# Kernel optimization log

Hardware: AMD Instinct MI355X
Metric: run time of the kernel (lower is better)

## Reference

```python
import jax, jax.numpy as jnp
import numpy as np

B = 16
N = [20000, 5000, 1250, 313, 79]          # node counts per pooling level (fine -> coarse)
E = [120000, 30000, 7500, 1878, 474]      # ~6 edges per node (triangle mesh)
FILTERS = [3, 32, 32, 64, 64, 64]
K = 6
Z = 64
COND = 2
N_LAYERS = 4


def setup_inputs():
    ks = iter(jax.random.split(jax.random.key(0), 64))
    inp = {}
    inp["x"] = jax.random.normal(next(ks), (B * N[0], FILTERS[0]), jnp.float32)
    inp["label"] = jax.random.normal(next(ks), (B, COND), jnp.float32)
    for i in range(5):
        inp[f"edges{i}"] = jax.random.randint(next(ks), (2, E[i]), 0, N[i])
    for i in range(4):
        inp[f"ds_idx{i}"] = jax.random.randint(next(ks), (N[i + 1],), 0, N[i])
        inp[f"us_idx{i}"] = jax.random.randint(next(ks), (N[i], 3), 0, N[i + 1])
        inp[f"us_w{i}"] = jax.random.uniform(next(ks), (N[i], 3), jnp.float32)
    for i in range(4):
        inp[f"enc_w{i}"] = 0.1 * jax.random.normal(next(ks), (K, FILTERS[i], FILTERS[i + 1]), jnp.float32)
        inp[f"enc_b{i}"] = 0.1 * jax.random.normal(next(ks), (FILTERS[i + 1],), jnp.float32)
    for i in range(5):
        inp[f"dec_w{i}"] = 0.1 * jax.random.normal(next(ks), (K, FILTERS[-i - 1], FILTERS[-i - 2]), jnp.float32)
    for i in range(4):
        inp[f"dec_b{i}"] = 0.1 * jax.random.normal(next(ks), (FILTERS[-i - 2],), jnp.float32)
    lat_in = N[4] * FILTERS[-1]
    inp["enc_mu_w"] = 0.1 * jax.random.normal(next(ks), (lat_in, Z), jnp.float32)
    inp["enc_mu_b"] = jnp.zeros((Z,), jnp.float32)
    inp["enc_lv_w"] = 0.1 * jax.random.normal(next(ks), (lat_in, Z), jnp.float32)
    inp["enc_lv_b"] = jnp.zeros((Z,), jnp.float32)
    inp["dec_lin_w"] = 0.1 * jax.random.normal(next(ks), (Z + COND, lat_in), jnp.float32)
    inp["dec_lin_b"] = jnp.zeros((lat_in,), jnp.float32)
    return inp


def _sym_norm(edges, n):
    # ChebConv_Coma.norm: norm = D^-1/2[row] * w * D^-1/2[col], unit weights
    row, col = edges[0], edges[1]
    deg = jnp.zeros((n,), jnp.float32).at[row].add(1.0)
    dinv = jnp.where(deg > 0, deg ** -0.5, 0.0)
    return dinv[row] * dinv[col]


def _cheb(x, edges, norm, W, b):
    # Chebyshev recursion: Tx_0=x, Tx_1=L~x, Tx_k=2 L~ Tx_{k-1} - Tx_{k-2}
    src, tgt = edges[0], edges[1]

    def prop(h):  # h: [B, Nn, F] -> scatter-sum of norm-weighted source features
        return jnp.zeros_like(h).at[:, tgt].add(h[:, src] * norm[None, :, None])

    Tx0 = x
    out = jnp.einsum('bnf,fg->bng', Tx0, W[0])
    Tx1 = prop(x)
    out = out + jnp.einsum('bnf,fg->bng', Tx1, W[1])
    for k in range(2, W.shape[0]):
        Tx2 = 2.0 * prop(Tx1) - Tx0
        out = out + jnp.einsum('bnf,fg->bng', Tx2, W[k])
        Tx0, Tx1 = Tx1, Tx2
    return out if b is None else out + b


def _forward(x, label, us_ws, enc_ws, enc_bs, dec_ws, dec_bs,
             enc_mu_w, enc_mu_b, enc_lv_w, enc_lv_b, dec_lin_w, dec_lin_b,
             edges, norms, ds_idx, us_idx):
    h = x.reshape(B, N[0], FILTERS[0])
    # encoder
    for i in range(N_LAYERS):
        h = jax.nn.relu(_cheb(h, edges[i], norms[i], enc_ws[i], enc_bs[i]))
        h = h[:, ds_idx[i]]  # binary downsample matrix == row gather
    h = h.reshape(B, N[4] * FILTERS[-1])
    mu = h @ enc_mu_w + enc_mu_b
    logvar = h @ enc_lv_w + enc_lv_b
    # reparameterize (fixed eps for determinism)
    eps = jax.random.normal(jax.random.key(42), mu.shape, mu.dtype)
    z = mu + eps * jnp.exp(0.5 * logvar)
    # decoder
    h = jnp.concatenate([z, label], axis=1)
    h = jax.nn.relu(h @ dec_lin_w + dec_lin_b).reshape(B, N[4], FILTERS[-1])
    for i in range(N_LAYERS):
        lvl = N_LAYERS - 1 - i
        # barycentric upsample: 3 nonzeros per output row
        h = jnp.einsum('rk,brkf->brf', us_ws[lvl], h[:, us_idx[lvl]])
        h = jax.nn.relu(_cheb(h, edges[lvl], norms[lvl], dec_ws[i], dec_bs[i]))
    # faithful quirk of the original: final conv uses A_edge_index[-1] (coarsest graph edges)
    h = _cheb(h, edges[-1], norms[-1], dec_ws[4], None)
    return h.reshape(-1, FILTERS[0]), mu, logvar


def reference(x, label,
              edges0, edges1, edges2, edges3, edges4,
              ds_idx0, ds_idx1, ds_idx2, ds_idx3,
              us_idx0, us_idx1, us_idx2, us_idx3,
              us_w0, us_w1, us_w2, us_w3,
              enc_w0, enc_w1, enc_w2, enc_w3,
              enc_b0, enc_b1, enc_b2, enc_b3,
              dec_w0, dec_w1, dec_w2, dec_w3, dec_w4,
              dec_b0, dec_b1, dec_b2, dec_b3,
              enc_mu_w, enc_mu_b, enc_lv_w, enc_lv_b, dec_lin_w, dec_lin_b):
    edges = [edges0, edges1, edges2, edges3, edges4]
    norms = [_sym_norm(edges[i], N[i]) for i in range(5)]
    return _forward(x, label,
                    [us_w0, us_w1, us_w2, us_w3],
                    [enc_w0, enc_w1, enc_w2, enc_w3],
                    [enc_b0, enc_b1, enc_b2, enc_b3],
                    [dec_w0, dec_w1, dec_w2, dec_w3, dec_w4],
                    [dec_b0, dec_b1, dec_b2, dec_b3],
                    enc_mu_w, enc_mu_b, enc_lv_w, enc_lv_b, dec_lin_w, dec_lin_b,
                    edges, norms,
                    [ds_idx0, ds_idx1, ds_idx2, ds_idx3],
                    [us_idx0, us_idx1, us_idx2, us_idx3])
```

## Files before the change

kernel.cpp:

```cpp
#include <hip/hip_runtime.h>
#include <cstdint>
#include <cstddef>

#define WG 256
#define NB 16


struct IP5 { const int* e[5]; };
struct Ptr3 { const float* p[3]; };


__global__ void k_zero_i(int* __restrict__ p, int n) {
  int i = blockIdx.x * WG + threadIdx.x;
  if (i < n) p[i] = 0;
}

__global__ void k_hist_all(IP5 ep, int* __restrict__ dsrc, int* __restrict__ dtgt) {
  int i = blockIdx.x * WG + threadIdx.x;
  if (i >= 159852) return;
  int l, eo, ee, no, co;
  if (i < 120000)      { l = 0; eo = 0;      ee = 120000; no = 0;     co = 0; }
  else if (i < 150000) { l = 1; eo = 120000; ee = 30000;  no = 20000; co = 20000; }
  else if (i < 157500) { l = 2; eo = 150000; ee = 7500;   no = 25000; co = 25000; }
  else if (i < 159378) { l = 3; eo = 157500; ee = 1878;   no = 26250; co = 26250; }
  else                 { l = 4; eo = 159378; ee = 474;    no = 26563; co = 26563; }
  int e = i - eo;
  const int* E = ep.e[l];
  atomicAdd(&dsrc[no + E[e]], 1);
  atomicAdd(&dtgt[co + E[ee + e]], 1);
}

__global__ void k_scan_all(const int* __restrict__ deg_all, int* __restrict__ rowptr_all,
                           int* __restrict__ cursor_all) {
  static const int Ns[5] = {20000, 5000, 1250, 313, 20000};
  static const int CO[5] = {0, 20000, 25000, 26250, 26563};
  static const int RO[5] = {0, 20001, 25002, 26253, 26567};
  __shared__ int s[WG];
  int l = blockIdx.x;
  int N = Ns[l];
  const int* deg = deg_all + CO[l];
  int* rowptr = rowptr_all + RO[l];
  int* cursor = cursor_all + CO[l];
  int t = threadIdx.x;
  int chunk = (N + WG - 1) / WG;
  int a = t * chunk;
  int b = min(N, a + chunk);
  int sum = 0;
  for (int i = a; i < b; i++) sum += deg[i];
  s[t] = sum;
  __syncthreads();
  for (int off = 1; off < WG; off <<= 1) {
    int v = (t >= off) ? s[t - off] : 0;
    __syncthreads();
    s[t] += v;
    __syncthreads();
  }
  int run = (t == 0) ? 0 : s[t - 1];
  for (int i = a; i < b; i++) {
    rowptr[i] = run;
    cursor[i] = run;
    run += deg[i];
  }
  if (t == 0) rowptr[N] = s[WG - 1];
}


static __device__ __forceinline__ float erfinv_f(float x) {
  float w = -log1pf(-x * x);
  float p;
  if (w < 5.0f) {
    w -= 2.5f;
    p = 2.81022636e-08f;
    p = fmaf(p, w, 3.43273939e-07f);
    p = fmaf(p, w, -3.5233877e-06f);
    p = fmaf(p, w, -4.39150654e-06f);
    p = fmaf(p, w, 0.00021858087f);
    p = fmaf(p, w, -0.00125372503f);
    p = fmaf(p, w, -0.00417768164f);
    p = fmaf(p, w, 0.246640727f);
    p = fmaf(p, w, 1.50140941f);
  } else {
    w = sqrtf(w) - 3.0f;
    p = -0.000200214257f;
    p = fmaf(p, w, 0.000100950558f);
    p = fmaf(p, w, 0.00134934322f);
    p = fmaf(p, w, -0.00367342844f);
    p = fmaf(p, w, 0.00573950773f);
    p = fmaf(p, w, -0.0076224613f);
    p = fmaf(p, w, 0.00943887047f);
    p = fmaf(p, w, 1.00167406f);
    p = fmaf(p, w, 2.83297682f);
  }
  return p * x;
}

static __device__ __forceinline__ float bits_to_normal(unsigned b) {
  float f = __uint_as_float((b >> 9) | 0x3f800000u) - 1.0f;
  const float lo = -0.99999994f;
  float u = f * (1.0f - lo) + lo;
  u = fmaxf(u, lo);
  return 1.41421356f * erfinv_f(u);
}

static __device__ __forceinline__ float eps_val(int i) {
  unsigned x0 = 0u, x1 = (unsigned)i;
  unsigned ks[3] = {0u, 42u, 0u ^ 42u ^ 0x1BD11BDAu};
  x0 += ks[0];
  x1 += ks[1];
  const int R[2][4] = {{13, 15, 26, 6}, {17, 29, 16, 24}};
#pragma unroll
  for (int it = 0; it < 5; it++) {
#pragma unroll
    for (int j = 0; j < 4; j++) {
      x0 += x1;
      int r = R[it & 1][j];
      x1 = (x1 << r) | (x1 >> (32 - r));
      x1 ^= x0;
    }
    x0 += ks[(it + 1) % 3];
    x1 += ks[(it + 2) % 3] + (unsigned)(it + 1);
  }
  return bits_to_normal(x0 ^ x1);
}

__global__ void k_fill_all(IP5 ep, const int* __restrict__ dsrc, int* __restrict__ cursor,
                           int* __restrict__ csrc, float* __restrict__ csw,
                           float* __restrict__ eps, const float* __restrict__ x,
                           float* __restrict__ sxl) {
  int blk = blockIdx.x;
  if (blk < 625) {
    int i = blk * WG + threadIdx.x;
    if (i >= 159852) return;
    int l, eo, ee, no, co, eb;
    if (i < 120000)      { l = 0; eo = 0;      ee = 120000; no = 0;     co = 0;     eb = 0; }
    else if (i < 150000) { l = 1; eo = 120000; ee = 30000;  no = 20000; co = 20000; eb = 120000; }
    else if (i < 157500) { l = 2; eo = 150000; ee = 7500;   no = 25000; co = 25000; eb = 150000; }
    else if (i < 159378) { l = 3; eo = 157500; ee = 1878;   no = 26250; co = 26250; eb = 157500; }
    else                 { l = 4; eo = 159378; ee = 474;    no = 26563; co = 26563; eb = 159378; }
    int e = i - eo;
    const int* E = ep.e[l];
    int s = E[e], t = E[ee + e];
    float da = (float)dsrc[no + s], db = (float)dsrc[no + t];
    float wa = (da > 0.f) ? (1.0f / sqrtf(da)) : 0.f;
    float wb = (db > 0.f) ? (1.0f / sqrtf(db)) : 0.f;
    int pos = atomicAdd(&cursor[co + t], 1);
    csrc[eb + pos] = s;
    csw[eb + pos] = wa * wb;
  } else if (blk < 629) {
    int j = (blk - 625) * WG + threadIdx.x;
    if (j < 1024) eps[j] = eps_val(j);
  } else {
    int j = (blk - 629) * WG + threadIdx.x;
    if (j >= NB * 20000 * 3) return;
    int f = j % 3;
    int b = (j / 3) % NB;
    int n = j / 48;
    sxl[j] = x[((size_t)b * 20000 + n) * 3 + f];
  }
}


#define RFL_I(v) __builtin_amdgcn_readfirstlane(v)
#define RFL_F(v) __int_as_float(__builtin_amdgcn_readfirstlane(__float_as_int(v)))

template <int F>
__global__ __launch_bounds__(WG) void k_propw(const float* __restrict__ in,
                                              float* __restrict__ out,
                                              const float* __restrict__ sub, float scale,
                                              const int* __restrict__ rowptr,
                                              const int* __restrict__ csrc,
                                              const float* __restrict__ csw, int N) {
  constexpr int C4 = F / 16;
  int node = blockIdx.x * 4 + (threadIdx.x >> 6);
  if (node >= N) return;
  int lane = threadIdx.x & 63;
  const float4* in4 = (const float4*)in;
  float4 acc[C4];
#pragma unroll
  for (int u = 0; u < C4; u++) acc[u] = make_float4(0.f, 0.f, 0.f, 0.f);
  int beg = rowptr[node], end = rowptr[node + 1];
  int j = beg;
  for (; j + 3 < end; j += 4) {
    int s0 = RFL_I(csrc[j]);
    int s1 = RFL_I(csrc[j + 1]);
    int s2 = RFL_I(csrc[j + 2]);
    int s3 = RFL_I(csrc[j + 3]);
    float w0 = RFL_F(csw[j]);
    float w1 = RFL_F(csw[j + 1]);
    float w2 = RFL_F(csw[j + 2]);
    float w3 = RFL_F(csw[j + 3]);
    const float4* p0 = in4 + (size_t)s0 * (4 * F) + lane;
    const float4* p1 = in4 + (size_t)s1 * (4 * F) + lane;
    const float4* p2 = in4 + (size_t)s2 * (4 * F) + lane;
    const float4* p3 = in4 + (size_t)s3 * (4 * F) + lane;
    float4 v0[C4], v1[C4], v2[C4], v3[C4];
#pragma unroll
    for (int u = 0; u < C4; u++) v0[u] = p0[u * 64];
#pragma unroll
    for (int u = 0; u < C4; u++) v1[u] = p1[u * 64];
#pragma unroll
    for (int u = 0; u < C4; u++) v2[u] = p2[u * 64];
#pragma unroll
    for (int u = 0; u < C4; u++) v3[u] = p3[u * 64];
#pragma unroll
    for (int u = 0; u < C4; u++) {
      acc[u].x = fmaf(w0, v0[u].x, acc[u].x); acc[u].y = fmaf(w0, v0[u].y, acc[u].y);
      acc[u].z = fmaf(w0, v0[u].z, acc[u].z); acc[u].w = fmaf(w0, v0[u].w, acc[u].w);
      acc[u].x = fmaf(w1, v1[u].x, acc[u].x); acc[u].y = fmaf(w1, v1[u].y, acc[u].y);
      acc[u].z = fmaf(w1, v1[u].z, acc[u].z); acc[u].w = fmaf(w1, v1[u].w, acc[u].w);
      acc[u].x = fmaf(w2, v2[u].x, acc[u].x); acc[u].y = fmaf(w2, v2[u].y, acc[u].y);
      acc[u].z = fmaf(w2, v2[u].z, acc[u].z); acc[u].w = fmaf(w2, v2[u].w, acc[u].w);
      acc[u].x = fmaf(w3, v3[u].x, acc[u].x); acc[u].y = fmaf(w3, v3[u].y, acc[u].y);
      acc[u].z = fmaf(w3, v3[u].z, acc[u].z); acc[u].w = fmaf(w3, v3[u].w, acc[u].w);
    }
  }
  for (; j < end; j++) {
    int s0 = RFL_I(csrc[j]);
    float w0 = RFL_F(csw[j]);
    const float4* p0 = in4 + (size_t)s0 * (4 * F) + lane;
#pragma unroll
    for (int u = 0; u < C4; u++) {
      float4 v0 = p0[u * 64];
      acc[u].x = fmaf(w0, v0.x, acc[u].x); acc[u].y = fmaf(w0, v0.y, acc[u].y);
      acc[u].z = fmaf(w0, v0.z, acc[u].z); acc[u].w = fmaf(w0, v0.w, acc[u].w);
    }
  }
  float4* o4 = (float4*)out + (size_t)node * (4 * F) + lane;
  if (sub) {
    const float4* s4 = (const float4*)sub + (size_t)node * (4 * F) + lane;
#pragma unroll
    for (int u = 0; u < C4; u++) {
      float4 sv = s4[u * 64];
      float4 r;
      r.x = fmaf(scale, acc[u].x, -sv.x); r.y = fmaf(scale, acc[u].y, -sv.y);
      r.z = fmaf(scale, acc[u].z, -sv.z); r.w = fmaf(scale, acc[u].w, -sv.w);
      o4[u * 64] = r;
    }
  } else {
#pragma unroll
    for (int u = 0; u < C4; u++) {
      float4 r;
      r.x = scale * acc[u].x; r.y = scale * acc[u].y;
      r.z = scale * acc[u].z; r.w = scale * acc[u].w;
      o4[u * 64] = r;
    }
  }
}

__global__ __launch_bounds__(WG) void k_propw3(const float* __restrict__ in,
                                               float* __restrict__ out,
                                               const float* __restrict__ sub, float scale,
                                               const int* __restrict__ rowptr,
                                               const int* __restrict__ csrc,
                                               const float* __restrict__ csw, int N) {
  int node = blockIdx.x * 4 + (threadIdx.x >> 6);
  if (node >= N) return;
  int lane = threadIdx.x & 63;
  if (lane >= 48) return;
  float acc = 0.f;
  int beg = rowptr[node], end = rowptr[node + 1];
  for (int j = beg; j < end; j++) {
    int s = RFL_I(csrc[j]);
    float w = RFL_F(csw[j]);
    acc = fmaf(w, in[(size_t)s * 48 + lane], acc);
  }
  float r = scale * acc;
  if (sub) r -= sub[(size_t)node * 48 + lane];
  out[(size_t)node * 48 + lane] = r;
}


template <int F, int G>
__global__ __launch_bounds__(WG) void k_gemm3(Ptr3 txs, const float* __restrict__ W,
                                              const float* __restrict__ bias,
                                              float* __restrict__ out, int rows,
                                              const int* __restrict__ idx,
                                              int accum, int relu) {
  constexpr int CG = G / 4;
  constexpr int RT = WG / CG;
  constexpr int RPB = RT * 4;
  __shared__ float sW[3 * F * G];
  for (int i = threadIdx.x; i < 3 * F * G; i += WG) sW[i] = W[i];
  __syncthreads();
  int cg = threadIdx.x % CG;
  int rt = threadIdx.x / CG;
  int row0 = blockIdx.x * RPB + rt * 4;
  if (row0 >= rows) return;
  size_t src0 = row0;
  if (idx) {
    int node = row0 >> 4, b = row0 & 15;
    src0 = (size_t)idx[node] * 16 + b;
  }
  float* o = out + (size_t)row0 * G + cg * 4;
  float4 acc[4];
  if (accum) {
#pragma unroll
    for (int r = 0; r < 4; r++) acc[r] = *(const float4*)(o + (size_t)r * G);
  } else if (bias) {
    float4 bv = *(const float4*)(bias + cg * 4);
#pragma unroll
    for (int r = 0; r < 4; r++) acc[r] = bv;
  } else {
#pragma unroll
    for (int r = 0; r < 4; r++) acc[r] = make_float4(0.f, 0.f, 0.f, 0.f);
  }
#pragma unroll
  for (int kk = 0; kk < 3; kk++) {
    const float* tb = txs.p[kk] + src0 * F;
    const float* w = sW + kk * F * G + cg * 4;
    if constexpr (F == 3) {
      float4 w0 = *(const float4*)(w + 0 * G);
      float4 w1 = *(const float4*)(w + 1 * G);
      float4 w2 = *(const float4*)(w + 2 * G);
#pragma unroll
      for (int r = 0; r < 4; r++) {
        float x0 = tb[r * 3 + 0], x1 = tb[r * 3 + 1], x2 = tb[r * 3 + 2];
        acc[r].x = fmaf(x0, w0.x, acc[r].x); acc[r].y = fmaf(x0, w0.y, acc[r].y);
        acc[r].z = fmaf(x0, w0.z, acc[r].z); acc[r].w = fmaf(x0, w0.w, acc[r].w);
        acc[r].x = fmaf(x1, w1.x, acc[r].x); acc[r].y = fmaf(x1, w1.y, acc[r].y);
        acc[r].z = fmaf(x1, w1.z, acc[r].z); acc[r].w = fmaf(x1, w1.w, acc[r].w);
        acc[r].x = fmaf(x2, w2.x, acc[r].x); acc[r].y = fmaf(x2, w2.y, acc[r].y);
        acc[r].z = fmaf(x2, w2.z, acc[r].z); acc[r].w = fmaf(x2, w2.w, acc[r].w);
      }
    } else {
#pragma unroll
      for (int fg = 0; fg < F / 4; fg++) {
        float4 xv[4];
#pragma unroll
        for (int r = 0; r < 4; r++) xv[r] = *(const float4*)(tb + (size_t)r * F + 4 * fg);
        float4 w0 = *(const float4*)(w + (4 * fg + 0) * G);
        float4 w1 = *(const float4*)(w + (4 * fg + 1) * G);
        float4 w2 = *(const float4*)(w + (4 * fg + 2) * G);
        float4 w3 = *(const float4*)(w + (4 * fg + 3) * G);
#pragma unroll
        for (int r = 0; r < 4; r++) {
          acc[r].x = fmaf(xv[r].x, w0.x, acc[r].x); acc[r].y = fmaf(xv[r].x, w0.y, acc[r].y);
          acc[r].z = fmaf(xv[r].x, w0.z, acc[r].z); acc[r].w = fmaf(xv[r].x, w0.w, acc[r].w);
          acc[r].x = fmaf(xv[r].y, w1.x, acc[r].x); acc[r].y = fmaf(xv[r].y, w1.y, acc[r].y);
          acc[r].z = fmaf(xv[r].y, w1.z, acc[r].z); acc[r].w = fmaf(xv[r].y, w1.w, acc[r].w);
          acc[r].x = fmaf(xv[r].z, w2.x, acc[r].x); acc[r].y = fmaf(xv[r].z, w2.y, acc[r].y);
          acc[r].z = fmaf(xv[r].z, w2.z, acc[r].z); acc[r].w = fmaf(xv[r].z, w2.w, acc[r].w);
          acc[r].x = fmaf(xv[r].w, w3.x, acc[r].x); acc[r].y = fmaf(xv[r].w, w3.y, acc[r].y);
          acc[r].z = fmaf(xv[r].w, w3.z, acc[r].z); acc[r].w = fmaf(xv[r].w, w3.w, acc[r].w);
        }
      }
    }
  }
  if (relu) {
#pragma unroll
    for (int r = 0; r < 4; r++) {
      acc[r].x = fmaxf(acc[r].x, 0.f); acc[r].y = fmaxf(acc[r].y, 0.f);
      acc[r].z = fmaxf(acc[r].z, 0.f); acc[r].w = fmaxf(acc[r].w, 0.f);
    }
  }
#pragma unroll
  for (int r = 0; r < 4; r++) *(float4*)(o + (size_t)r * G) = acc[r];
}

__global__ __launch_bounds__(WG) void k_gemm3_final(Ptr3 txs, const float* __restrict__ W,
                                                    const float* __restrict__ W4,
                                                    float* __restrict__ out,
                                                    float* __restrict__ dout, int rows) {
  constexpr int F = 32, G = 32;
  constexpr int CG = 8, RT = 32, RPB = 128;
  __shared__ float sW[3 * F * G];
  __shared__ float sWc[96];
  for (int i = threadIdx.x; i < 3 * F * G; i += WG) sW[i] = W[i];
  if (threadIdx.x < 96)
    sWc[threadIdx.x] = W4[threadIdx.x] - W4[192 + threadIdx.x] + W4[384 + threadIdx.x];
  __syncthreads();
  int cg = threadIdx.x % CG;
  int rt = threadIdx.x / CG;
  int row0 = blockIdx.x * RPB + rt * 4;
  float* o = out + (size_t)row0 * G + cg * 4;
  float4 acc[4];
#pragma unroll
  for (int r = 0; r < 4; r++) acc[r] = *(const float4*)(o + (size_t)r * G);
#pragma unroll
  for (int kk = 0; kk < 3; kk++) {
    const float* tb = txs.p[kk] + (size_t)row0 * F;
    const float* w = sW + kk * F * G + cg * 4;
#pragma unroll
    for (int fg = 0; fg < F / 4; fg++) {
      float4 xv[4];
#pragma unroll
      for (int r = 0; r < 4; r++) xv[r] = *(const float4*)(tb + (size_t)r * F + 4 * fg);
      float4 w0 = *(const float4*)(w + (4 * fg + 0) * G);
      float4 w1 = *(const float4*)(w + (4 * fg + 1) * G);
      float4 w2 = *(const float4*)(w + (4 * fg + 2) * G);
      float4 w3 = *(const float4*)(w + (4 * fg + 3) * G);
#pragma unroll
      for (int r = 0; r < 4; r++) {
        acc[r].x = fmaf(xv[r].x, w0.x, acc[r].x); acc[r].y = fmaf(xv[r].x, w0.y, acc[r].y);
        acc[r].z = fmaf(xv[r].x, w0.z, acc[r].z); acc[r].w = fmaf(xv[r].x, w0.w, acc[r].w);
        acc[r].x = fmaf(xv[r].y, w1.x, acc[r].x); acc[r].y = fmaf(xv[r].y, w1.y, acc[r].y);
        acc[r].z = fmaf(xv[r].y, w1.z, acc[r].z); acc[r].w = fmaf(xv[r].y, w1.w, acc[r].w);
        acc[r].x = fmaf(xv[r].z, w2.x, acc[r].x); acc[r].y = fmaf(xv[r].z, w2.y, acc[r].y);
        acc[r].z = fmaf(xv[r].z, w2.z, acc[r].z); acc[r].w = fmaf(xv[r].z, w2.w, acc[r].w);
        acc[r].x = fmaf(xv[r].w, w3.x, acc[r].x); acc[r].y = fmaf(xv[r].w, w3.y, acc[r].y);
        acc[r].z = fmaf(xv[r].w, w3.z, acc[r].z); acc[r].w = fmaf(xv[r].w, w3.w, acc[r].w);
      }
    }
  }
#pragma unroll
  for (int r = 0; r < 4; r++) {
    acc[r].x = fmaxf(acc[r].x, 0.f); acc[r].y = fmaxf(acc[r].y, 0.f);
    acc[r].z = fmaxf(acc[r].z, 0.f); acc[r].w = fmaxf(acc[r].w, 0.f);
  }
  if ((row0 >> 4) < 79) {
#pragma unroll
    for (int r = 0; r < 4; r++) *(float4*)(o + (size_t)r * G) = acc[r];
  }
#pragma unroll
  for (int r = 0; r < 4; r++) {
    float av[4] = {acc[r].x, acc[r].y, acc[r].z, acc[r].w};
    float p0 = 0.f, p1 = 0.f, p2 = 0.f;
#pragma unroll
    for (int j = 0; j < 4; j++) {
      int f = cg * 4 + j;
      p0 = fmaf(av[j], sWc[f * 3 + 0], p0);
      p1 = fmaf(av[j], sWc[f * 3 + 1], p1);
      p2 = fmaf(av[j], sWc[f * 3 + 2], p2);
    }
#pragma unroll
    for (int m = 4; m >= 1; m >>= 1) {
      p0 += __shfl_xor(p0, m, 64);
      p1 += __shfl_xor(p1, m, 64);
      p2 += __shfl_xor(p2, m, 64);
    }
    if (cg == 0) {
      int row = row0 + r;
      int n = row >> 4, b = row & 15;
      float* od = dout + ((size_t)b * 20000 + n) * 3;
      od[0] = p0; od[1] = p1; od[2] = p2;
    }
  }
}

__global__ __launch_bounds__(256) void k_final_fix(const float* __restrict__ in,
                                                   const float* __restrict__ W,
                                                   const int* __restrict__ rowptr,
                                                   const int* __restrict__ csrc,
                                                   const float* __restrict__ csw,
                                                   float* __restrict__ out) {
  __shared__ float B0[79 * 32], B1[79 * 32], B2[79 * 32];
  __shared__ float sacc[79 * 3];
  __shared__ float sW[576];
  int b = blockIdx.x, t = threadIdx.x;
  for (int i = t; i < 576; i += 256) sW[i] = W[i];
  for (int i = t; i < 2528; i += 256) {
    int r = i >> 5, f = i & 31;
    B0[i] = in[((size_t)r * 16 + b) * 32 + f];
  }
  __syncthreads();
  for (int i = t; i < 237; i += 256) {
    int r = i / 3, g = i % 3;
    float a = 0.f;
    for (int f = 0; f < 32; f++) a = fmaf(B0[r * 32 + f], sW[f * 3 + g], a);
    sacc[i] = a;
  }
  for (int i = t; i < 2528; i += 256) {
    int r = i >> 5, f = i & 31;
    float a = 0.f;
    for (int j = rowptr[r]; j < rowptr[r + 1]; j++) a = fmaf(csw[j], B0[csrc[j] * 32 + f], a);
    B1[i] = a;
  }
  __syncthreads();
  for (int i = t; i < 237; i += 256) {
    int r = i / 3, g = i % 3;
    float a = sacc[i];
    for (int f = 0; f < 32; f++) a = fmaf(B1[r * 32 + f], sW[96 + f * 3 + g], a);
    sacc[i] = a;
  }
  for (int i = t; i < 2528; i += 256) {
    int r = i >> 5, f = i & 31;
    float a = 0.f;
    for (int j = rowptr[r]; j < rowptr[r + 1]; j++) a = fmaf(csw[j], B1[csrc[j] * 32 + f], a);
    B2[i] = 2.f * a - B0[i];
  }
  __syncthreads();
  for (int i = t; i < 237; i += 256) {
    int r = i / 3, g = i % 3;
    float a = sacc[i];
    for (int f = 0; f < 32; f++) a = fmaf(B2[r * 32 + f], sW[192 + f * 3 + g], a);
    sacc[i] = a;
  }
  __syncthreads();
  for (int i = t; i < 2528; i += 256) {
    int r = i >> 5, f = i & 31;
    float a = 0.f;
    for (int j = rowptr[r]; j < rowptr[r + 1]; j++) a = fmaf(csw[j], B2[csrc[j] * 32 + f], a);
    B0[i] = 2.f * a - B1[i];
  }
  __syncthreads();
  for (int i = t; i < 237; i += 256) {
    int r = i / 3, g = i % 3;
    float a = sacc[i];
    for (int f = 0; f < 32; f++) a = fmaf(B0[r * 32 + f], sW[288 + f * 3 + g], a);
    sacc[i] = a;
  }
  __syncthreads();
  for (int i = t; i < 2528; i += 256) {
    int r = i >> 5, f = i & 31;
    float a = 0.f;
    for (int j = rowptr[r]; j < rowptr[r + 1]; j++) a = fmaf(csw[j], B0[csrc[j] * 32 + f], a);
    B1[i] = 2.f * a - B2[i];
  }
  __syncthreads();
  for (int i = t; i < 237; i += 256) {
    int r = i / 3, g = i % 3;
    float a = sacc[i];
    for (int f = 0; f < 32; f++) a = fmaf(B1[r * 32 + f], sW[384 + f * 3 + g], a);
    sacc[i] = a;
  }
  __syncthreads();
  for (int i = t; i < 2528; i += 256) {
    int r = i >> 5, f = i & 31;
    float a = 0.f;
    for (int j = rowptr[r]; j < rowptr[r + 1]; j++) a = fmaf(csw[j], B1[csrc[j] * 32 + f], a);
    B2[i] = 2.f * a - B0[i];
  }
  __syncthreads();
  for (int i = t; i < 237; i += 256) {
    int r = i / 3, g = i % 3;
    float a = sacc[i];
    for (int f = 0; f < 32; f++) a = fmaf(B2[r * 32 + f], sW[480 + f * 3 + g], a);
    out[((size_t)b * 20000 + r) * 3 + g] = a;
  }
}

template <int F>
__global__ __launch_bounds__(WG) void k_us(const float* __restrict__ in,
                                           float* __restrict__ out,
                                           const int* __restrict__ uidx,
                                           const float* __restrict__ uw, int Nf) {
  int i = blockIdx.x * WG + threadIdx.x;
  int total = Nf * NB * F;
  if (i >= total) return;
  int pos = i % (NB * F);
  int r = i / (NB * F);
  float acc = 0.f;
#pragma unroll
  for (int k = 0; k < 3; k++) {
    float v = in[(size_t)uidx[r * 3 + k] * NB * F + pos];
    acc = fmaf(uw[r * 3 + k], fmaxf(v, 0.f), acc);
  }
  out[i] = acc;
}


__global__ __launch_bounds__(64) void k_latent(const float* __restrict__ h,
                                               const float* __restrict__ muW,
                                               const float* __restrict__ muB,
                                               const float* __restrict__ lvW,
                                               const float* __restrict__ lvB,
                                               const float* __restrict__ eps,
                                               const float* __restrict__ label,
                                               float* __restrict__ mu_out,
                                               float* __restrict__ lv_out,
                                               float* __restrict__ hcat) {
  int b = blockIdx.x / 64;
  int g = blockIdx.x % 64;
  int l = threadIdx.x;
  float am = 0.f, al = 0.f;
  for (int i = l; i < 5056; i += 64) {
    int n = i >> 6, f = i & 63;
    float hv = h[(size_t)(n * 16 + b) * 64 + f];
    am = fmaf(hv, muW[(size_t)i * 64 + g], am);
    al = fmaf(hv, lvW[(size_t)i * 64 + g], al);
  }
  for (int off = 32; off > 0; off >>= 1) {
    am += __shfl_down(am, off, 64);
    al += __shfl_down(al, off, 64);
  }
  if (l == 0) {
    am += muB[g];
    al += lvB[g];
    mu_out[b * 64 + g] = am;
    lv_out[b * 64 + g] = al;
    hcat[b * 66 + g] = fmaf(eps[b * 64 + g], expf(0.5f * al), am);
    if (g < 2) hcat[b * 66 + 64 + g] = label[b * 2 + g];
  }
}

__global__ __launch_bounds__(WG) void k_declin(const float* __restrict__ hcat,
                                               const float* __restrict__ W,
                                               const float* __restrict__ bias,
                                               float* __restrict__ out) {
  int idx = blockIdx.x * WG + threadIdx.x;
  if (idx >= NB * 5056) return;
  int b = idx / 5056, j = idx % 5056;
  int n = j >> 6, f = j & 63;
  float acc = bias[j];
  const float* hc = hcat + b * 66;
#pragma unroll
  for (int i = 0; i < 66; i++) acc = fmaf(hc[i], W[(size_t)i * 5056 + j], acc);
  out[(size_t)(n * 16 + b) * 64 + f] = fmaxf(acc, 0.f);
}


static inline dim3 grid1(long n) { return dim3((unsigned)((n + WG - 1) / WG)); }

template <int F, int G>
static void run_cheb(float* in, float* out, float* A, float* B,
                     const float* W, const float* bias, int N, int Nout,
                     const int* ds_idx, int relu_last,
                     const int* rowptr, const int* csrc, const float* csw,
                     hipStream_t st) {
  int orows = NB * Nout;
  constexpr int RPB = (WG / (G / 4)) * 4;
  dim3 gG((unsigned)((orows + RPB - 1) / RPB));
  dim3 gP((unsigned)((N + 3) / 4));
  int relu2 = ds_idx ? 1 : relu_last;
  if constexpr (F == 3) {
    k_propw3<<<gP, WG, 0, st>>>(in, A, nullptr, 1.f, rowptr, csrc, csw, N);
    k_propw3<<<gP, WG, 0, st>>>(A, B, in, 2.f, rowptr, csrc, csw, N);
    Ptr3 p1{{in, A, B}};
    k_gemm3<F, G><<<gG, WG, 0, st>>>(p1, W, bias, out, orows, ds_idx, 0, 0);
    k_propw3<<<gP, WG, 0, st>>>(B, in, A, 2.f, rowptr, csrc, csw, N);
    k_propw3<<<gP, WG, 0, st>>>(in, A, B, 2.f, rowptr, csrc, csw, N);
    k_propw3<<<gP, WG, 0, st>>>(A, B, in, 2.f, rowptr, csrc, csw, N);
    Ptr3 p2{{in, A, B}};
    k_gemm3<F, G><<<gG, WG, 0, st>>>(p2, W + 3 * F * G, nullptr, out, orows, ds_idx, 1, relu2);
  } else {
    k_propw<F><<<gP, WG, 0, st>>>(in, A, nullptr, 1.f, rowptr, csrc, csw, N);
    k_propw<F><<<gP, WG, 0, st>>>(A, B, in, 2.f, rowptr, csrc, csw, N);
    Ptr3 p1{{in, A, B}};
    k_gemm3<F, G><<<gG, WG, 0, st>>>(p1, W, bias, out, orows, ds_idx, 0, 0);
    k_propw<F><<<gP, WG, 0, st>>>(B, in, A, 2.f, rowptr, csrc, csw, N);
    k_propw<F><<<gP, WG, 0, st>>>(in, A, B, 2.f, rowptr, csrc, csw, N);
    k_propw<F><<<gP, WG, 0, st>>>(A, B, in, 2.f, rowptr, csrc, csw, N);
    Ptr3 p2{{in, A, B}};
    k_gemm3<F, G><<<gG, WG, 0, st>>>(p2, W + 3 * F * G, nullptr, out, orows, ds_idx, 1, relu2);
  }
}

extern "C" void kernel_launch(void* const* d_in, const int* in_sizes, int n_in,
                              void* d_out, int out_size, void* d_ws, size_t ws_size,
                              hipStream_t stream) {
  const float* x = (const float*)d_in[0];
  const float* label = (const float*)d_in[1];
  IP5 ep;
  for (int l = 0; l < 5; l++) ep.e[l] = (const int*)d_in[2 + l];
  const int* ds_idx[4];
  const int* us_idx[4];
  const float* us_w[4];
  for (int i = 0; i < 4; i++) {
    ds_idx[i] = (const int*)d_in[7 + 3 * i];
    us_idx[i] = (const int*)d_in[8 + 3 * i];
    us_w[i] = (const float*)d_in[9 + 3 * i];
  }
  const float* enc_w[4];
  const float* enc_b[4];
  for (int i = 0; i < 4; i++) {
    enc_w[i] = (const float*)d_in[19 + 2 * i];
    enc_b[i] = (const float*)d_in[20 + 2 * i];
  }
  const float* dec_w[5];
  for (int i = 0; i < 5; i++) dec_w[i] = (const float*)d_in[27 + i];
  const float* dec_b[4];
  for (int i = 0; i < 4; i++) dec_b[i] = (const float*)d_in[32 + i];
  const float* mu_w = (const float*)d_in[36];
  const float* mu_b = (const float*)d_in[37];
  const float* lv_w = (const float*)d_in[38];
  const float* lv_b = (const float*)d_in[39];
  const float* dl_w = (const float*)d_in[40];
  const float* dl_b = (const float*)d_in[41];

  float* wsf = (float*)d_ws;
  size_t off = 0;
  auto carve = [&](size_t n) -> float* {
    float* p = wsf + off;
    off += (n + 63) & ~(size_t)63;
    return p;
  };
  const size_t SLOT = 10240000;
  float* s0 = carve(SLOT);
  float* s1 = carve(SLOT);
  float* s2 = carve(SLOT);
  float* s3 = carve(SLOT);
  float* sxl = carve(960000);
  int* deg_all = (int*)carve(26642 + 46563);
  int* deg_src_all = deg_all;
  int* deg_tgt_all = deg_all + 26642;
  int* rowptr_all = (int*)carve(46568);
  int* cursor_all = (int*)carve(46563);
  int* csrc_all = (int*)carve(159852);
  float* csw_all = carve(159852);
  float* eps = carve(1024);
  float* hcat = carve(1056);

  static const int ROFF[5] = {0, 20001, 25002, 26253, 26567};
  static const int EOFF[5] = {0, 120000, 150000, 157500, 159378};
  auto RP = [&](int l) { return rowptr_all + ROFF[l]; };
  auto CS = [&](int l) { return csrc_all + EOFF[l]; };
  auto CW = [&](int l) { return csw_all + EOFF[l]; };

  k_zero_i<<<grid1(26642 + 46563), WG, 0, stream>>>(deg_all, 26642 + 46563);
  k_hist_all<<<grid1(159852), WG, 0, stream>>>(ep, deg_src_all, deg_tgt_all);
  k_scan_all<<<5, WG, 0, stream>>>(deg_tgt_all, rowptr_all, cursor_all);
  k_fill_all<<<625 + 4 + 3750, WG, 0, stream>>>(ep, deg_src_all, cursor_all, csrc_all,
                                                csw_all, eps, x, sxl);

  float* mu_out = (float*)d_out + 960000;
  float* lv_out = (float*)d_out + 961024;

  run_cheb<3, 32>(sxl, s1, s2, s3, enc_w[0], enc_b[0], 20000, 5000, ds_idx[0], 0,
                  RP(0), CS(0), CW(0), stream);
  run_cheb<32, 32>(s1, s0, s2, s3, enc_w[1], enc_b[1], 5000, 1250, ds_idx[1], 0,
                   RP(1), CS(1), CW(1), stream);
  run_cheb<32, 64>(s0, s1, s2, s3, enc_w[2], enc_b[2], 1250, 313, ds_idx[2], 0,
                   RP(2), CS(2), CW(2), stream);
  run_cheb<64, 64>(s1, s0, s2, s3, enc_w[3], enc_b[3], 313, 79, ds_idx[3], 0,
                   RP(3), CS(3), CW(3), stream);

  k_latent<<<1024, 64, 0, stream>>>(s0, mu_w, mu_b, lv_w, lv_b, eps, label, mu_out, lv_out, hcat);
  k_declin<<<grid1(NB * 5056), WG, 0, stream>>>(hcat, dl_w, dl_b, s0);

  k_us<64><<<grid1((long)313 * NB * 64), WG, 0, stream>>>(s0, s1, us_idx[3], us_w[3], 313);
  run_cheb<64, 64>(s1, s0, s2, s3, dec_w[0], dec_b[0], 313, 313, nullptr, 0,
                   RP(3), CS(3), CW(3), stream);
  k_us<64><<<grid1((long)1250 * NB * 64), WG, 0, stream>>>(s0, s1, us_idx[2], us_w[2], 1250);
  run_cheb<64, 64>(s1, s0, s2, s3, dec_w[1], dec_b[1], 1250, 1250, nullptr, 0,
                   RP(2), CS(2), CW(2), stream);
  k_us<64><<<grid1((long)5000 * NB * 64), WG, 0, stream>>>(s0, s1, us_idx[1], us_w[1], 5000);
  run_cheb<64, 32>(s1, s0, s2, s3, dec_w[2], dec_b[2], 5000, 5000, nullptr, 0,
                   RP(1), CS(1), CW(1), stream);
  k_us<32><<<grid1((long)20000 * NB * 32), WG, 0, stream>>>(s0, s1, us_idx[0], us_w[0], 20000);

  {
    const int N = 20000;
    int rows = NB * N;
    dim3 gP((unsigned)((N + 3) / 4));
    dim3 gG((unsigned)(rows / 128));
    k_propw<32><<<gP, WG, 0, stream>>>(s1, s2, nullptr, 1.f, RP(0), CS(0), CW(0), N);
    k_propw<32><<<gP, WG, 0, stream>>>(s2, s3, s1, 2.f, RP(0), CS(0), CW(0), N);
    Ptr3 p1{{s1, s2, s3}};
    dim3 gG1((unsigned)(rows / 128));
    k_gemm3<32, 32><<<gG1, WG, 0, stream>>>(p1, dec_w[3], dec_b[3], s0, rows, nullptr, 0, 0);
    k_propw<32><<<gP, WG, 0, stream>>>(s3, s1, s2, 2.f, RP(0), CS(0), CW(0), N);
    k_propw<32><<<gP, WG, 0, stream>>>(s1, s2, s3, 2.f, RP(0), CS(0), CW(0), N);
    k_propw<32><<<gP, WG, 0, stream>>>(s2, s3, s1, 2.f, RP(0), CS(0), CW(0), N);
    Ptr3 p2{{s1, s2, s3}};
    k_gemm3_final<<<gG, WG, 0, stream>>>(p2, dec_w[3] + 3 * 32 * 32, dec_w[4], s0,
                                         (float*)d_out, rows);
  }

  k_final_fix<<<16, 256, 0, stream>>>(s0, dec_w[4], RP(4), CS(4), CW(4), (float*)d_out);
}
```

Baseline: 1.333 ms.

## Use monomial powers of L instead of Chebyshev recursion via precombined weights

```diff
diff --git a/kernel.cpp b/kernel.cpp
--- a/kernel.cpp
+++ b/kernel.cpp
@@ -8,6 +8,12 @@
 
 struct IP5 { const int* e[5]; };
 struct Ptr3 { const float* p[3]; };
+struct WComb { const float* w[8]; float* c[8]; };
+
+static __device__ __forceinline__ void fma4(float4& a, float s, const float4& b) {
+  a.x = fmaf(s, b.x, a.x); a.y = fmaf(s, b.y, a.y);
+  a.z = fmaf(s, b.z, a.z); a.w = fmaf(s, b.w, a.w);
+}
 
 
 __global__ void k_zero_i(int* __restrict__ p, int n) {
@@ -62,6 +68,26 @@
     run += deg[i];
   }
   if (t == 0) rowptr[N] = s[WG - 1];
+}
+
+__global__ void k_combine(WComb wc) {
+  static const int M[8] = {96, 1024, 2048, 4096, 4096, 4096, 2048, 1024};
+  static const int OFF[8] = {0, 96, 1120, 3168, 7264, 11360, 15456, 17504};
+  int i = blockIdx.x * WG + threadIdx.x;
+  if (i >= 18528) return;
+  int l = 0;
+  while (l < 7 && i >= OFF[l + 1]) l++;
+  int e = i - OFF[l], m = M[l];
+  const float* w = wc.w[l];
+  float* c = wc.c[l];
+  float w0 = w[e], w1 = w[m + e], w2 = w[2 * m + e];
+  float w3 = w[3 * m + e], w4 = w[4 * m + e], w5 = w[5 * m + e];
+  c[e]         = w0 - w2 + w4;
+  c[m + e]     = w1 - 3.f * w3 + 5.f * w5;
+  c[2 * m + e] = 2.f * w2 - 8.f * w4;
+  c[3 * m + e] = 4.f * w3 - 20.f * w5;
+  c[4 * m + e] = 8.f * w4;
+  c[5 * m + e] = 16.f * w5;
 }
 
 
@@ -166,7 +192,6 @@
 template <int F>
 __global__ __launch_bounds__(WG) void k_propw(const float* __restrict__ in,
                                               float* __restrict__ out,
-                                              const float* __restrict__ sub, float scale,
                                               const int* __restrict__ rowptr,
                                               const int* __restrict__ csrc,
                                               const float* __restrict__ csw, int N) {
@@ -204,14 +229,10 @@
     for (int u = 0; u < C4; u++) v3[u] = p3[u * 64];
 #pragma unroll
     for (int u = 0; u < C4; u++) {
-      acc[u].x = fmaf(w0, v0[u].x, acc[u].x); acc[u].y = fmaf(w0, v0[u].y, acc[u].y);
-      acc[u].z = fmaf(w0, v0[u].z, acc[u].z); acc[u].w = fmaf(w0, v0[u].w, acc[u].w);
-      acc[u].x = fmaf(w1, v1[u].x, acc[u].x); acc[u].y = fmaf(w1, v1[u].y, acc[u].y);
-      acc[u].z = fmaf(w1, v1[u].z, acc[u].z); acc[u].w = fmaf(w1, v1[u].w, acc[u].w);
-      acc[u].x = fmaf(w2, v2[u].x, acc[u].x); acc[u].y = fmaf(w2, v2[u].y, acc[u].y);
-      acc[u].z = fmaf(w2, v2[u].z, acc[u].z); acc[u].w = fmaf(w2, v2[u].w, acc[u].w);
-      acc[u].x = fmaf(w3, v3[u].x, acc[u].x); acc[u].y = fmaf(w3, v3[u].y, acc[u].y);
-      acc[u].z = fmaf(w3, v3[u].z, acc[u].z); acc[u].w = fmaf(w3, v3[u].w, acc[u].w);
+      fma4(acc[u], w0, v0[u]);
+      fma4(acc[u], w1, v1[u]);
+      fma4(acc[u], w2, v2[u]);
+      fma4(acc[u], w3, v3[u]);
     }
   }
   for (; j < end; j++) {
@@ -221,35 +242,16 @@
 #pragma unroll
     for (int u = 0; u < C4; u++) {
       float4 v0 = p0[u * 64];
-      acc[u].x = fmaf(w0, v0.x, acc[u].x); acc[u].y = fmaf(w0, v0.y, acc[u].y);
-      acc[u].z = fmaf(w0, v0.z, acc[u].z); acc[u].w = fmaf(w0, v0.w, acc[u].w);
+      fma4(acc[u], w0, v0);
     }
   }
   float4* o4 = (float4*)out + (size_t)node * (4 * F) + lane;
-  if (sub) {
-    const float4* s4 = (const float4*)sub + (size_t)node * (4 * F) + lane;
-#pragma unroll
-    for (int u = 0; u < C4; u++) {
-      float4 sv = s4[u * 64];
-      float4 r;
-      r.x = fmaf(scale, acc[u].x, -sv.x); r.y = fmaf(scale, acc[u].y, -sv.y);
-      r.z = fmaf(scale, acc[u].z, -sv.z); r.w = fmaf(scale, acc[u].w, -sv.w);
-      o4[u * 64] = r;
-    }
-  } else {
-#pragma unroll
-    for (int u = 0; u < C4; u++) {
-      float4 r;
-      r.x = scale * acc[u].x; r.y = scale * acc[u].y;
-      r.z = scale * acc[u].z; r.w = scale * acc[u].w;
-      o4[u * 64] = r;
-    }
-  }
+#pragma unroll
+  for (int u = 0; u < C4; u++) o4[u * 64] = acc[u];
 }
 
 __global__ __launch_bounds__(WG) void k_propw3(const float* __restrict__ in,
                                                float* __restrict__ out,
-                                               const float* __restrict__ sub, float scale,
                                                const int* __restrict__ rowptr,
                                                const int* __restrict__ csrc,
                                                const float* __restrict__ csw, int N) {
@@ -264,9 +266,7 @@
     float w = RFL_F(csw[j]);
     acc = fmaf(w, in[(size_t)s * 48 + lane], acc);
   }
-  float r = scale * acc;
-  if (sub) r -= sub[(size_t)node * 48 + lane];
-  out[(size_t)node * 48 + lane] = r;
+  out[(size_t)node * 48 + lane] = acc;
 }
 
 
@@ -315,12 +315,9 @@
 #pragma unroll
       for (int r = 0; r < 4; r++) {
         float x0 = tb[r * 3 + 0], x1 = tb[r * 3 + 1], x2 = tb[r * 3 + 2];
-        acc[r].x = fmaf(x0, w0.x, acc[r].x); acc[r].y = fmaf(x0, w0.y, acc[r].y);
-        acc[r].z = fmaf(x0, w0.z, acc[r].z); acc[r].w = fmaf(x0, w0.w, acc[r].w);
-        acc[r].x = fmaf(x1, w1.x, acc[r].x); acc[r].y = fmaf(x1, w1.y, acc[r].y);
-        acc[r].z = fmaf(x1, w1.z, acc[r].z); acc[r].w = fmaf(x1, w1.w, acc[r].w);
-        acc[r].x = fmaf(x2, w2.x, acc[r].x); acc[r].y = fmaf(x2, w2.y, acc[r].y);
-        acc[r].z = fmaf(x2, w2.z, acc[r].z); acc[r].w = fmaf(x2, w2.w, acc[r].w);
+        fma4(acc[r], x0, w0);
+        fma4(acc[r], x1, w1);
+        fma4(acc[r], x2, w2);
       }
     } else {
 #pragma unroll
@@ -334,14 +331,10 @@
         float4 w3 = *(const float4*)(w + (4 * fg + 3) * G);
 #pragma unroll
         for (int r = 0; r < 4; r++) {
-          acc[r].x = fmaf(xv[r].x, w0.x, acc[r].x); acc[r].y = fmaf(xv[r].x, w0.y, acc[r].y);
-          acc[r].z = fmaf(xv[r].x, w0.z, acc[r].z); acc[r].w = fmaf(xv[r].x, w0.w, acc[r].w);
-          acc[r].x = fmaf(xv[r].y, w1.x, acc[r].x); acc[r].y = fmaf(xv[r].y, w1.y, acc[r].y);
-          acc[r].z = fmaf(xv[r].y, w1.z, acc[r].z); acc[r].w = fmaf(xv[r].y, w1.w, acc[r].w);
-          acc[r].x = fmaf(xv[r].z, w2.x, acc[r].x); acc[r].y = fmaf(xv[r].z, w2.y, acc[r].y);
-          acc[r].z = fmaf(xv[r].z, w2.z, acc[r].z); acc[r].w = fmaf(xv[r].z, w2.w, acc[r].w);
-          acc[r].x = fmaf(xv[r].w, w3.x, acc[r].x); acc[r].y = fmaf(xv[r].w, w3.y, acc[r].y);
-          acc[r].z = fmaf(xv[r].w, w3.z, acc[r].z); acc[r].w = fmaf(xv[r].w, w3.w, acc[r].w);
+          fma4(acc[r], xv[r].x, w0);
+          fma4(acc[r], xv[r].y, w1);
+          fma4(acc[r], xv[r].z, w2);
+          fma4(acc[r], xv[r].w, w3);
         }
       }
     }
@@ -362,7 +355,7 @@
                                                     float* __restrict__ out,
                                                     float* __restrict__ dout, int rows) {
   constexpr int F = 32, G = 32;
-  constexpr int CG = 8, RT = 32, RPB = 128;
+  constexpr int CG = 8, RPB = 128;
   __shared__ float sW[3 * F * G];
   __shared__ float sWc[96];
   for (int i = threadIdx.x; i < 3 * F * G; i += WG) sW[i] = W[i];
@@ -391,14 +384,10 @@
       float4 w3 = *(const float4*)(w + (4 * fg + 3) * G);
 #pragma unroll
       for (int r = 0; r < 4; r++) {
-        acc[r].x = fmaf(xv[r].x, w0.x, acc[r].x); acc[r].y = fmaf(xv[r].x, w0.y, acc[r].y);
-        acc[r].z = fmaf(xv[r].x, w0.z, acc[r].z); acc[r].w = fmaf(xv[r].x, w0.w, acc[r].w);
-        acc[r].x = fmaf(xv[r].y, w1.x, acc[r].x); acc[r].y = fmaf(xv[r].y, w1.y, acc[r].y);
-        acc[r].z = fmaf(xv[r].y, w1.z, acc[r].z); acc[r].w = fmaf(xv[r].y, w1.w, acc[r].w);
-        acc[r].x = fmaf(xv[r].z, w2.x, acc[r].x); acc[r].y = fmaf(xv[r].z, w2.y, acc[r].y);
-        acc[r].z = fmaf(xv[r].z, w2.z, acc[r].z); acc[r].w = fmaf(xv[r].z, w2.w, acc[r].w);
-        acc[r].x = fmaf(xv[r].w, w3.x, acc[r].x); acc[r].y = fmaf(xv[r].w, w3.y, acc[r].y);
-        acc[r].z = fmaf(xv[r].w, w3.z, acc[r].z); acc[r].w = fmaf(xv[r].w, w3.w, acc[r].w);
+        fma4(acc[r], xv[r].x, w0);
+        fma4(acc[r], xv[r].y, w1);
+        fma4(acc[r], xv[r].z, w2);
+        fma4(acc[r], xv[r].w, w3);
       }
     }
   }
@@ -603,35 +592,35 @@
 
 template <int F, int G>
 static void run_cheb(float* in, float* out, float* A, float* B,
-                     const float* W, const float* bias, int N, int Nout,
+                     const float* C, const float* bias, int N, int Nout,
                      const int* ds_idx, int relu_last,
                      const int* rowptr, const int* csrc, const float* csw,
                      hipStream_t st) {
   int orows = NB * Nout;
+  dim3 gP((unsigned)((N + 3) / 4));
   constexpr int RPB = (WG / (G / 4)) * 4;
   dim3 gG((unsigned)((orows + RPB - 1) / RPB));
-  dim3 gP((unsigned)((N + 3) / 4));
   int relu2 = ds_idx ? 1 : relu_last;
   if constexpr (F == 3) {
-    k_propw3<<<gP, WG, 0, st>>>(in, A, nullptr, 1.f, rowptr, csrc, csw, N);
-    k_propw3<<<gP, WG, 0, st>>>(A, B, in, 2.f, rowptr, csrc, csw, N);
+    k_propw3<<<gP, WG, 0, st>>>(in, A, rowptr, csrc, csw, N);
+    k_propw3<<<gP, WG, 0, st>>>(A, B, rowptr, csrc, csw, N);
     Ptr3 p1{{in, A, B}};
-    k_gemm3<F, G><<<gG, WG, 0, st>>>(p1, W, bias, out, orows, ds_idx, 0, 0);
-    k_propw3<<<gP, WG, 0, st>>>(B, in, A, 2.f, rowptr, csrc, csw, N);
-    k_propw3<<<gP, WG, 0, st>>>(in, A, B, 2.f, rowptr, csrc, csw, N);
-    k_propw3<<<gP, WG, 0, st>>>(A, B, in, 2.f, rowptr, csrc, csw, N);
+    k_gemm3<F, G><<<gG, WG, 0, st>>>(p1, C, bias, out, orows, ds_idx, 0, 0);
+    k_propw3<<<gP, WG, 0, st>>>(B, in, rowptr, csrc, csw, N);
+    k_propw3<<<gP, WG, 0, st>>>(in, A, rowptr, csrc, csw, N);
+    k_propw3<<<gP, WG, 0, st>>>(A, B, rowptr, csrc, csw, N);
     Ptr3 p2{{in, A, B}};
-    k_gemm3<F, G><<<gG, WG, 0, st>>>(p2, W + 3 * F * G, nullptr, out, orows, ds_idx, 1, relu2);
+    k_gemm3<F, G><<<gG, WG, 0, st>>>(p2, C + 3 * F * G, nullptr, out, orows, ds_idx, 1, relu2);
   } else {
-    k_propw<F><<<gP, WG, 0, st>>>(in, A, nullptr, 1.f, rowptr, csrc, csw, N);
-    k_propw<F><<<gP, WG, 0, st>>>(A, B, in, 2.f, rowptr, csrc, csw, N);
+    k_propw<F><<<gP, WG, 0, st>>>(in, A, rowptr, csrc, csw, N);
+    k_propw<F><<<gP, WG, 0, st>>>(A, B, rowptr, csrc, csw, N);
     Ptr3 p1{{in, A, B}};
-    k_gemm3<F, G><<<gG, WG, 0, st>>>(p1, W, bias, out, orows, ds_idx, 0, 0);
-    k_propw<F><<<gP, WG, 0, st>>>(B, in, A, 2.f, rowptr, csrc, csw, N);
-    k_propw<F><<<gP, WG, 0, st>>>(in, A, B, 2.f, rowptr, csrc, csw, N);
-    k_propw<F><<<gP, WG, 0, st>>>(A, B, in, 2.f, rowptr, csrc, csw, N);
+    k_gemm3<F, G><<<gG, WG, 0, st>>>(p1, C, bias, out, orows, ds_idx, 0, 0);
+    k_propw<F><<<gP, WG, 0, st>>>(B, in, rowptr, csrc, csw, N);
+    k_propw<F><<<gP, WG, 0, st>>>(in, A, rowptr, csrc, csw, N);
+    k_propw<F><<<gP, WG, 0, st>>>(A, B, rowptr, csrc, csw, N);
     Ptr3 p2{{in, A, B}};
-    k_gemm3<F, G><<<gG, WG, 0, st>>>(p2, W + 3 * F * G, nullptr, out, orows, ds_idx, 1, relu2);
+    k_gemm3<F, G><<<gG, WG, 0, st>>>(p2, C + 3 * F * G, nullptr, out, orows, ds_idx, 1, relu2);
   }
 }
 
@@ -689,6 +678,9 @@
   float* csw_all = carve(159852);
   float* eps = carve(1024);
   float* hcat = carve(1056);
+  static const int CM[8] = {96, 1024, 2048, 4096, 4096, 4096, 2048, 1024};
+  float* comb[8];
+  for (int l = 0; l < 8; l++) comb[l] = carve((size_t)6 * CM[l]);
 
   static const int ROFF[5] = {0, 20001, 25002, 26253, 26567};
   static const int EOFF[5] = {0, 120000, 150000, 157500, 159378};
@@ -701,30 +693,36 @@
   k_scan_all<<<5, WG, 0, stream>>>(deg_tgt_all, rowptr_all, cursor_all);
   k_fill_all<<<625 + 4 + 3750, WG, 0, stream>>>(ep, deg_src_all, cursor_all, csrc_all,
                                                 csw_all, eps, x, sxl);
+  {
+    WComb wc;
+    for (int l = 0; l < 4; l++) { wc.w[l] = enc_w[l]; wc.c[l] = comb[l]; }
+    for (int l = 0; l < 4; l++) { wc.w[4 + l] = dec_w[l]; wc.c[4 + l] = comb[4 + l]; }
+    k_combine<<<grid1(18528), WG, 0, stream>>>(wc);
+  }
 
   float* mu_out = (float*)d_out + 960000;
   float* lv_out = (float*)d_out + 961024;
 
-  run_cheb<3, 32>(sxl, s1, s2, s3, enc_w[0], enc_b[0], 20000, 5000, ds_idx[0], 0,
+  run_cheb<3, 32>(sxl, s1, s2, s3, comb[0], enc_b[0], 20000, 5000, ds_idx[0], 0,
                   RP(0), CS(0), CW(0), stream);
-  run_cheb<32, 32>(s1, s0, s2, s3, enc_w[1], enc_b[1], 5000, 1250, ds_idx[1], 0,
+  run_cheb<32, 32>(s1, s0, s2, s3, comb[1], enc_b[1], 5000, 1250, ds_idx[1], 0,
                    RP(1), CS(1), CW(1), stream);
-  run_cheb<32, 64>(s0, s1, s2, s3, enc_w[2], enc_b[2], 1250, 313, ds_idx[2], 0,
+  run_cheb<32, 64>(s0, s1, s2, s3, comb[2], enc_b[2], 1250, 313, ds_idx[2], 0,
                    RP(2), CS(2), CW(2), stream);
-  run_cheb<64, 64>(s1, s0, s2, s3, enc_w[3], enc_b[3], 313, 79, ds_idx[3], 0,
+  run_cheb<64, 64>(s1, s0, s2, s3, comb[3], enc_b[3], 313, 79, ds_idx[3], 0,
                    RP(3), CS(3), CW(3), stream);
 
   k_latent<<<1024, 64, 0, stream>>>(s0, mu_w, mu_b, lv_w, lv_b, eps, label, mu_out, lv_out, hcat);
   k_declin<<<grid1(NB * 5056), WG, 0, stream>>>(hcat, dl_w, dl_b, s0);
 
   k_us<64><<<grid1((long)313 * NB * 64), WG, 0, stream>>>(s0, s1, us_idx[3], us_w[3], 313);
-  run_cheb<64, 64>(s1, s0, s2, s3, dec_w[0], dec_b[0], 313, 313, nullptr, 0,
+  run_cheb<64, 64>(s1, s0, s2, s3, comb[4], dec_b[0], 313, 313, nullptr, 0,
                    RP(3), CS(3), CW(3), stream);
   k_us<64><<<grid1((long)1250 * NB * 64), WG, 0, stream>>>(s0, s1, us_idx[2], us_w[2], 1250);
-  run_cheb<64, 64>(s1, s0, s2, s3, dec_w[1], dec_b[1], 1250, 1250, nullptr, 0,
+  run_cheb<64, 64>(s1, s0, s2, s3, comb[5], dec_b[1], 1250, 1250, nullptr, 0,
                    RP(2), CS(2), CW(2), stream);
   k_us<64><<<grid1((long)5000 * NB * 64), WG, 0, stream>>>(s0, s1, us_idx[1], us_w[1], 5000);
-  run_cheb<64, 32>(s1, s0, s2, s3, dec_w[2], dec_b[2], 5000, 5000, nullptr, 0,
+  run_cheb<64, 32>(s1, s0, s2, s3, comb[6], dec_b[2], 5000, 5000, nullptr, 0,
                    RP(1), CS(1), CW(1), stream);
   k_us<32><<<grid1((long)20000 * NB * 32), WG, 0, stream>>>(s0, s1, us_idx[0], us_w[0], 20000);
 
@@ -733,16 +731,15 @@
     int rows = NB * N;
     dim3 gP((unsigned)((N + 3) / 4));
     dim3 gG((unsigned)(rows / 128));
-    k_propw<32><<<gP, WG, 0, stream>>>(s1, s2, nullptr, 1.f, RP(0), CS(0), CW(0), N);
-    k_propw<32><<<gP, WG, 0, stream>>>(s2, s3, s1, 2.f, RP(0), CS(0), CW(0), N);
+    k_propw<32><<<gP, WG, 0, stream>>>(s1, s2, RP(0), CS(0), CW(0), N);
+    k_propw<32><<<gP, WG, 0, stream>>>(s2, s3, RP(0), CS(0), CW(0), N);
     Ptr3 p1{{s1, s2, s3}};
-    dim3 gG1((unsigned)(rows / 128));
-    k_gemm3<32, 32><<<gG1, WG, 0, stream>>>(p1, dec_w[3], dec_b[3], s0, rows, nullptr, 0, 0);
-    k_propw<32><<<gP, WG, 0, stream>>>(s3, s1, s2, 2.f, RP(0), CS(0), CW(0), N);
-    k_propw<32><<<gP, WG, 0, stream>>>(s1, s2, s3, 2.f, RP(0), CS(0), CW(0), N);
-    k_propw<32><<<gP, WG, 0, stream>>>(s2, s3, s1, 2.f, RP(0), CS(0), CW(0), N);
+    k_gemm3<32, 32><<<gG, WG, 0, stream>>>(p1, comb[7], dec_b[3], s0, rows, nullptr, 0, 0);
+    k_propw<32><<<gP, WG, 0, stream>>>(s3, s1, RP(0), CS(0), CW(0), N);
+    k_propw<32><<<gP, WG, 0, stream>>>(s1, s2, RP(0), CS(0), CW(0), N);
+    k_propw<32><<<gP, WG, 0, stream>>>(s2, s3, RP(0), CS(0), CW(0), N);
     Ptr3 p2{{s1, s2, s3}};
-    k_gemm3_final<<<gG, WG, 0, stream>>>(p2, dec_w[3] + 3 * 32 * 32, dec_w[4], s0,
+    k_gemm3_final<<<gG, WG, 0, stream>>>(p2, comb[7] + 3 * 32 * 32, dec_w[4], s0,
                                          (float*)d_out, rows);
   }
 
```

Measured after the change: 1.200 ms. 10.0% less time.
